# Kernel optimization log

Hardware: AMD Instinct MI355X
Metric: run time of the kernel (lower is better)

## Reference

```python
import jax, jax.numpy as jnp
import numpy as np

B = 4        # number of point clouds (equal-size contiguous batches)
P = 8192     # points per cloud
C_IN = 64
C_OUT = 64
K = 16       # kNN neighbors (includes the point itself, as in PyG knn)
EPS = 1e-5
NEG_SLOPE = 0.2


def setup_inputs() -> dict:
    key = jax.random.key(0)
    k1, k2, k3 = jax.random.split(key, 3)
    x = jax.random.normal(k1, (B * P, C_IN), dtype=jnp.float32)
    batch = jnp.repeat(jnp.arange(B, dtype=jnp.int64), P)  # sorted, equal sizes
    W = jax.random.normal(k2, (2 * C_IN, C_OUT), dtype=jnp.float32) * (1.0 / np.sqrt(2 * C_IN))
    b = jax.random.normal(k3, (C_OUT,), dtype=jnp.float32) * 0.01
    gamma = jnp.ones((C_OUT,), dtype=jnp.float32)
    beta = jnp.zeros((C_OUT,), dtype=jnp.float32)
    return {"x": x, "batch": batch, "W": W, "b": b, "gamma": gamma, "beta": beta}


def _edgeconv(x, W, b, gamma, beta):
    xb = x.reshape(B, P, C_IN)
    # per-cloud pairwise squared distances: [B, P, P]
    sq = jnp.sum(xb * xb, axis=-1)
    d = sq[:, :, None] + sq[:, None, :] - 2.0 * jnp.einsum("bpc,bqc->bpq", xb, xb)
    # k nearest neighbors (smallest distance, self included)
    _, idx = jax.lax.top_k(-d, K)                      # [B, P, K]
    xj = jax.vmap(lambda pts, ind: pts[ind])(xb, idx)  # [B, P, K, C_IN]
    xi = xb[:, :, None, :]
    e = jnp.concatenate([jnp.broadcast_to(xi, xj.shape), xj - xi], axis=-1)  # [B,P,K,2C]
    # edge MLP: Linear -> BatchNorm1d (training-mode batch stats over all edges) -> LeakyReLU
    h = jnp.einsum("bpke,eo->bpko", e, W) + b          # [B, P, K, C_OUT]
    hf = h.reshape(-1, C_OUT)
    mean = jnp.mean(hf, axis=0)
    var = jnp.mean(hf * hf, axis=0) - mean * mean      # biased variance (torch BN)
    hn = (h - mean) * jax.lax.rsqrt(var + EPS) * gamma + beta
    a = jnp.where(hn >= 0, hn, NEG_SLOPE * hn)
    # max aggregation over neighbors
    return jnp.max(a, axis=2).reshape(B * P, C_OUT)


def reference(x, batch, W, b, gamma, beta):
    # `batch` encodes B equal-size contiguous clouds; kNN is computed per cloud.
    return _edgeconv(x, W, b, gamma, beta)
```

## Files before the change

### kernel.cpp

```cpp
#include <hip/hip_runtime.h>
#include <cfloat>

#define BATCH 4
#define P 8192
#define C 64
#define KNN 16
#define NPTS (BATCH * P)
#define NEDGE (NPTS * KNN)
#define EPSV 1e-5f
#define SLOPE 0.2f
#define CAP 16

typedef __attribute__((ext_vector_type(8))) short bf16x8;
typedef __attribute__((ext_vector_type(16))) float f32x16;


__device__ __forceinline__ unsigned short f2bf(float f) {
    unsigned u = __float_as_uint(f);
    u += 0x7FFFu + ((u >> 16) & 1u);
    return (unsigned short)(u >> 16);
}
__device__ __forceinline__ float bf2f(unsigned short s) {
    return __uint_as_float(((unsigned)s) << 16);
}

__global__ void prep_frag(const float* __restrict__ x, uint4* __restrict__ xfh,
                          uint4* __restrict__ xfm, uint4* __restrict__ xfl,
                          float* __restrict__ sq) {
    __shared__ float part[32][9];
    int tid = threadIdx.x;
    int ptl = tid >> 3, j8 = tid & 7;
    int g = blockIdx.x;
    int p = g * 32 + ptl;
    const float4* xp = (const float4*)(x + (size_t)p * C + j8 * 8);
    float4 a = xp[0], b = xp[1];
    float v[8] = {a.x, a.y, a.z, a.w, b.x, b.y, b.z, b.w};
    unsigned short hs[8], ms[8], ls[8];
    float ssum = 0.f;
#pragma unroll
    for (int e = 0; e < 8; ++e) {
        float xv = v[e];
        ssum = fmaf(xv, xv, ssum);
        unsigned short h = f2bf(xv);
        float r1 = xv - bf2f(h);
        unsigned short m = f2bf(r1);
        float r2 = r1 - bf2f(m);
        unsigned short l = f2bf(r2);
        hs[e] = h; ms[e] = m; ls[e] = l;
    }
    int dst = (g * 4 + (j8 >> 1)) * 64 + ptl + 32 * (j8 & 1);
    uint4 ph, pm, pl;
    ph.x = (unsigned)hs[0] | ((unsigned)hs[1] << 16);
    ph.y = (unsigned)hs[2] | ((unsigned)hs[3] << 16);
    ph.z = (unsigned)hs[4] | ((unsigned)hs[5] << 16);
    ph.w = (unsigned)hs[6] | ((unsigned)hs[7] << 16);
    pm.x = (unsigned)ms[0] | ((unsigned)ms[1] << 16);
    pm.y = (unsigned)ms[2] | ((unsigned)ms[3] << 16);
    pm.z = (unsigned)ms[4] | ((unsigned)ms[5] << 16);
    pm.w = (unsigned)ms[6] | ((unsigned)ms[7] << 16);
    pl.x = (unsigned)ls[0] | ((unsigned)ls[1] << 16);
    pl.y = (unsigned)ls[2] | ((unsigned)ls[3] << 16);
    pl.z = (unsigned)ls[4] | ((unsigned)ls[5] << 16);
    pl.w = (unsigned)ls[6] | ((unsigned)ls[7] << 16);
    xfh[dst] = ph; xfm[dst] = pm; xfl[dst] = pl;
    part[ptl][j8] = ssum;
    __syncthreads();
    if (j8 == 0) {
        float s = 0.f;
#pragma unroll
        for (int k = 0; k < 8; ++k) s += part[ptl][k];
        sq[p] = s;
    }
}

__device__ __forceinline__ void tk_insert(float (&v)[16], int (&id)[16],
                                          float& worst, float s, int cand) {
    if (s < worst) {
        float w = v[0];
        int pos = 0;
#pragma unroll
        for (int j = 1; j < 16; ++j) {
            bool g = v[j] > w;
            w = g ? v[j] : w;
            pos = g ? j : pos;
        }
#pragma unroll
        for (int j = 0; j < 16; ++j) {
            if (j == pos) { v[j] = s; id[j] = cand; }
        }
        float nw = v[0];
#pragma unroll
        for (int j = 1; j < 16; ++j) nw = fmaxf(nw, v[j]);
        worst = nw;
    }
}

__global__ __launch_bounds__(256, 2) void knn_kernel(const uint4* __restrict__ xfh,
                                                     const uint4* __restrict__ xfm,
                                                     const uint4* __restrict__ xfl,
                                                     const float* __restrict__ sq,
                                                     int* __restrict__ idx_out) {
    __shared__ float scoresL[64 * 65];
    __shared__ float bufv[64 * 17];
    __shared__ int   bufi[64 * 17];
    __shared__ int   cntL[64];
    __shared__ float worstL[64];

    int tid = threadIdx.x;
    int b = blockIdx.x & 3;
    int tile = blockIdx.x >> 2;
    int bglob = b * P;
    int r0 = tile * 64;
    int w = tid >> 6, lane = tid & 63;
    int wr = w & 1, wc = w >> 1;

    if (tid < 64) { cntL[tid] = 0; worstL[tid] = FLT_MAX; }

    int gA = ((bglob + r0) >> 5) + wr;
    bf16x8 Ah[4], Am[4], Al[4];
#pragma unroll
    for (int kk = 0; kk < 4; ++kk) {
        Ah[kk] = __builtin_bit_cast(bf16x8, xfh[(gA * 4 + kk) * 64 + lane]);
        Am[kk] = __builtin_bit_cast(bf16x8, xfm[(gA * 4 + kk) * 64 + lane]);
        Al[kk] = __builtin_bit_cast(bf16x8, xfl[(gA * 4 + kk) * 64 + lane]);
    }

    float tv[16];
    int ti[16];
    float worst = FLT_MAX;
#pragma unroll
    for (int j = 0; j < 16; ++j) { tv[j] = FLT_MAX; ti[j] = 0; }
    int rown = ((lane & 15) << 2) | w;
    bool owner = (lane < 16);

    int selr = tid & 63;
    int selq = tid >> 6;

    for (int chunk = 0; chunk < P / 64; ++chunk) {
        int c0 = chunk * 64;
        int gB = ((bglob + c0) >> 5) + wc;
        bf16x8 Bh[4], Bm[4], Bl[4];
#pragma unroll
        for (int kk = 0; kk < 4; ++kk) {
            Bh[kk] = __builtin_bit_cast(bf16x8, xfh[(gB * 4 + kk) * 64 + lane]);
            Bm[kk] = __builtin_bit_cast(bf16x8, xfm[(gB * 4 + kk) * 64 + lane]);
            Bl[kk] = __builtin_bit_cast(bf16x8, xfl[(gB * 4 + kk) * 64 + lane]);
        }
        float sc = sq[bglob + c0 + wc * 32 + (lane & 31)];

        f32x16 acc0, acc1;
#pragma unroll
        for (int i = 0; i < 16; ++i) { acc0[i] = 0.f; acc1[i] = 0.f; }
#pragma unroll
        for (int kk = 0; kk < 4; ++kk) {
            acc0 = __builtin_amdgcn_mfma_f32_32x32x16_bf16(Ah[kk], Bh[kk], acc0, 0, 0, 0);
            acc1 = __builtin_amdgcn_mfma_f32_32x32x16_bf16(Ah[kk], Bm[kk], acc1, 0, 0, 0);
            acc0 = __builtin_amdgcn_mfma_f32_32x32x16_bf16(Am[kk], Bh[kk], acc0, 0, 0, 0);
            acc1 = __builtin_amdgcn_mfma_f32_32x32x16_bf16(Am[kk], Bm[kk], acc1, 0, 0, 0);
            acc0 = __builtin_amdgcn_mfma_f32_32x32x16_bf16(Ah[kk], Bl[kk], acc0, 0, 0, 0);
            acc1 = __builtin_amdgcn_mfma_f32_32x32x16_bf16(Al[kk], Bh[kk], acc1, 0, 0, 0);
        }

        __syncthreads();
        {
            int colL = wc * 32 + (lane & 31);
            int rbase = wr * 32 + 4 * (lane >> 5);
#pragma unroll
            for (int reg = 0; reg < 16; ++reg) {
                int row = rbase + (reg & 3) + 8 * (reg >> 2);
                scoresL[row * 65 + colL] = fmaf(-2.f, acc0[reg] + acc1[reg], sc);
            }
        }
        __syncthreads();
        {
            float wst = worstL[selr];
#pragma unroll
            for (int j = 0; j < 16; ++j) {
                float s = scoresL[selr * 65 + selq * 16 + j];
                if (s < wst) {
                    int slot = atomicAdd(&cntL[selr], 1);
                    if (slot < CAP) {
                        bufv[selr * 17 + slot] = s;
                        bufi[selr * 17 + slot] = c0 + selq * 16 + j;
                    }
                }
            }
        }
        __syncthreads();
        if (owner) {
            int n = cntL[rown];
            if (n > 0) {
                if (n > CAP) {
                    for (int e = 0; e < 64; ++e)
                        tk_insert(tv, ti, worst, scoresL[rown * 65 + e], c0 + e);
                } else {
                    for (int k = 0; k < n; ++k)
                        tk_insert(tv, ti, worst, bufv[rown * 17 + k], bufi[rown * 17 + k]);
                }
                cntL[rown] = 0;
                worstL[rown] = worst;
            }
        }
    }

    if (owner) {
        size_t o = ((size_t)(bglob + r0 + rown)) * KNN;
#pragma unroll
        for (int j = 0; j < 16; ++j) idx_out[o + j] = bglob + ti[j];
    }
}

__global__ void prep_UV(const float* __restrict__ x, const float* __restrict__ W,
                        float* __restrict__ U, float* __restrict__ V) {
    __shared__ float Ws[128][64];
    __shared__ float xs[4][64];
    int tid = threadIdx.x;
    for (int i = tid; i < 128 * 64; i += 256) ((float*)Ws)[i] = W[i];
    int p0 = blockIdx.x * 4;
    int r = tid >> 6, c = tid & 63;
    xs[r][c] = x[(size_t)(p0 + r) * C + c];
    __syncthreads();
    float u = 0.f, v = 0.f;
#pragma unroll
    for (int k = 0; k < 64; ++k) {
        float xv = xs[r][k];
        float w1 = Ws[k][c];
        float w2 = Ws[64 + k][c];
        u = fmaf(xv, w1 - w2, u);
        v = fmaf(xv, w2, v);
    }
    size_t o = (size_t)(p0 + r) * C + c;
    U[o] = u;
    V[o] = v;
}

__global__ void stats_kernel(const float* __restrict__ U, const float* __restrict__ V,
                             const float* __restrict__ bias, const int* __restrict__ idx,
                             float* __restrict__ stats) {
    int tid = threadIdx.x;
    int c = tid & 63, kk = tid >> 6;
    int p0 = blockIdx.x * 32;
    float bc = bias[c];
    float sum = 0.f, sumsq = 0.f;
    for (int pp = 0; pp < 32; ++pp) {
        int p = p0 + pp;
        float u = U[(size_t)p * C + c] + bc;
#pragma unroll
        for (int k4 = 0; k4 < 4; ++k4) {
            int j = idx[(size_t)p * KNN + kk * 4 + k4];
            float h = u + V[(size_t)j * C + c];
            sum += h;
            sumsq = fmaf(h, h, sumsq);
        }
    }
    __shared__ float red[2][4][64];
    red[0][kk][c] = sum;
    red[1][kk][c] = sumsq;
    __syncthreads();
    if (tid < 64) {
        float s = red[0][0][tid] + red[0][1][tid] + red[0][2][tid] + red[0][3][tid];
        atomicAdd(&stats[tid], s);
    } else if (tid < 128) {
        int cc = tid - 64;
        float s = red[1][0][cc] + red[1][1][cc] + red[1][2][cc] + red[1][3][cc];
        atomicAdd(&stats[64 + cc], s);
    }
}

__global__ void finalize_kernel(const float* __restrict__ stats,
                                const float* __restrict__ gamma,
                                const float* __restrict__ beta,
                                float* __restrict__ sshift) {
    int c = threadIdx.x;
    const float N = (float)NEDGE;
    float mean = stats[c] / N;
    float var = stats[64 + c] / N - mean * mean;
    float s = gamma[c] * rsqrtf(var + EPSV);
    sshift[c] = s;
    sshift[64 + c] = beta[c] - mean * s;
}

__global__ void out_kernel(const float* __restrict__ U, const float* __restrict__ V,
                           const float* __restrict__ bias, const int* __restrict__ idx,
                           const float* __restrict__ sshift, float* __restrict__ out) {
    int tid = threadIdx.x;
    int c = tid & 63, g = tid >> 6;
    int p0 = blockIdx.x * 16;
    float s = sshift[c], t = sshift[64 + c];
    float bc = bias[c];
    for (int pp = g; pp < 16; pp += 4) {
        int p = p0 + pp;
        float mx = -FLT_MAX, mn = FLT_MAX;
#pragma unroll
        for (int k = 0; k < KNN; ++k) {
            int j = idx[(size_t)p * KNN + k];
            float v = V[(size_t)j * C + c];
            mx = fmaxf(mx, v);
            mn = fminf(mn, v);
        }
        float hsel = (s >= 0.f) ? mx : mn;
        float hn = fmaf(s, U[(size_t)p * C + c] + bc + hsel, t);
        out[(size_t)p * C + c] = (hn >= 0.f) ? hn : SLOPE * hn;
    }
}

extern "C" void kernel_launch(void* const* d_in, const int* in_sizes, int n_in,
                              void* d_out, int out_size, void* d_ws, size_t ws_size,
                              hipStream_t stream) {
    const float* x     = (const float*)d_in[0];
    const float* W     = (const float*)d_in[2];
    const float* bias  = (const float*)d_in[3];
    const float* gamma = (const float*)d_in[4];
    const float* beta  = (const float*)d_in[5];
    float* out = (float*)d_out;

    float* wsf    = (float*)d_ws;
    float* U      = wsf;
    float* V      = wsf + 2097152;
    uint4* xfh    = (uint4*)wsf;
    uint4* xfm    = (uint4*)(wsf + 1048576);
    uint4* xfl    = (uint4*)(wsf + 2097152);
    float* sq     = wsf + 4194304;
    float* stats  = wsf + 4227072;
    float* sshift = wsf + 4227200;
    int*   idx    = (int*)(wsf + 4227328);

    hipLaunchKernelGGL(prep_frag, dim3(NPTS / 32), dim3(256), 0, stream, x, xfh, xfm, xfl, sq);
    hipLaunchKernelGGL(knn_kernel, dim3(BATCH * (P / 64)), dim3(256), 0, stream,
                       (const uint4*)xfh, (const uint4*)xfm, (const uint4*)xfl, sq, idx);
    hipLaunchKernelGGL(prep_UV, dim3(NPTS / 4), dim3(256), 0, stream, x, W, U, V);
    hipMemsetAsync(stats, 0, 128 * sizeof(float), stream);
    hipLaunchKernelGGL(stats_kernel, dim3(NPTS / 32), dim3(256), 0, stream, U, V, bias, idx, stats);
    hipLaunchKernelGGL(finalize_kernel, dim3(1), dim3(64), 0, stream, stats, gamma, beta, sshift);
    hipLaunchKernelGGL(out_kernel, dim3(NPTS / 16), dim3(256), 0, stream, U, V, bias, idx, sshift, out);
}
```

Measured before the change: 590.1 us.

## Split kNN column range into quarters and merge partial top-k lists

The kNN kernel now splits each row tile's candidate columns into four quarters, each handled by its own block. Each block writes a partial top-16 of distances and indices to workspace, and a new merge kernel combines the four partial lists per point. The grid before had only 512 blocks, which underfilled the GPU, so this raises the block count fourfold, and launch bounds are raised to allow more resident blocks. The cost is an extra kernel launch, extra global traffic for the partial lists, and possible register pressure from the tighter launch bound.

```diff
diff --git a/kernel.cpp b/kernel.cpp
--- a/kernel.cpp
+++ b/kernel.cpp
@@ -10,6 +10,8 @@
 #define EPSV 1e-5f
 #define SLOPE 0.2f
 #define CAP 16
+#define NQ 4
+#define QCOLS (P / NQ)
 
 typedef __attribute__((ext_vector_type(8))) short bf16x8;
 typedef __attribute__((ext_vector_type(16))) float f32x16;
@@ -95,11 +97,12 @@
     }
 }
 
-__global__ __launch_bounds__(256, 2) void knn_kernel(const uint4* __restrict__ xfh,
+__global__ __launch_bounds__(256, 6) void knn_kernel(const uint4* __restrict__ xfh,
                                                      const uint4* __restrict__ xfm,
                                                      const uint4* __restrict__ xfl,
                                                      const float* __restrict__ sq,
-                                                     int* __restrict__ idx_out) {
+                                                     float* __restrict__ pv,
+                                                     int* __restrict__ pi) {
     __shared__ float scoresL[64 * 65];
     __shared__ float bufv[64 * 17];
     __shared__ int   bufi[64 * 17];
@@ -108,9 +111,12 @@
 
     int tid = threadIdx.x;
     int b = blockIdx.x & 3;
-    int tile = blockIdx.x >> 2;
+    int t = blockIdx.x >> 2;
+    int tile = t & 127;
+    int quarter = t >> 7;
     int bglob = b * P;
     int r0 = tile * 64;
+    int colbase = quarter * QCOLS;
     int w = tid >> 6, lane = tid & 63;
     int wr = w & 1, wc = w >> 1;
 
@@ -136,8 +142,8 @@
     int selr = tid & 63;
     int selq = tid >> 6;
 
-    for (int chunk = 0; chunk < P / 64; ++chunk) {
-        int c0 = chunk * 64;
+    for (int chunk = 0; chunk < QCOLS / 64; ++chunk) {
+        int c0 = colbase + chunk * 64;
         int gB = ((bglob + c0) >> 5) + wc;
         bf16x8 Bh[4], Bm[4], Bl[4];
 #pragma unroll
@@ -204,9 +210,40 @@
     }
 
     if (owner) {
-        size_t o = ((size_t)(bglob + r0 + rown)) * KNN;
-#pragma unroll
-        for (int j = 0; j < 16; ++j) idx_out[o + j] = bglob + ti[j];
+        size_t o = (((size_t)(bglob + r0 + rown)) * NQ + quarter) * KNN;
+#pragma unroll
+        for (int j = 0; j < 16; ++j) {
+            pv[o + j] = tv[j];
+            pi[o + j] = bglob + ti[j];
+        }
+    }
+}
+
+__global__ void merge_kernel(const float* __restrict__ pv, const int* __restrict__ pi,
+                             int* __restrict__ idx_out) {
+    __shared__ float mv[64][65];
+    __shared__ int   mi[64][65];
+    int tid = threadIdx.x;
+    int lr = tid & 63, q = tid >> 6;
+    int row = blockIdx.x * 64 + lr;
+    size_t o = ((size_t)row * NQ + q) * KNN;
+#pragma unroll
+    for (int j = 0; j < 16; ++j) {
+        mv[lr][q * 16 + j] = pv[o + j];
+        mi[lr][q * 16 + j] = pi[o + j];
+    }
+    __syncthreads();
+    if (tid < 64) {
+        float tv[16];
+        int ti[16];
+        float worst = FLT_MAX;
+#pragma unroll
+        for (int j = 0; j < 16; ++j) { tv[j] = FLT_MAX; ti[j] = 0; }
+        for (int e = 0; e < 64; ++e)
+            tk_insert(tv, ti, worst, mv[tid][e], mi[tid][e]);
+        size_t oo = (size_t)row * KNN;
+#pragma unroll
+        for (int j = 0; j < 16; ++j) idx_out[oo + j] = ti[j];
     }
 }
 
@@ -324,10 +361,13 @@
     float* stats  = wsf + 4227072;
     float* sshift = wsf + 4227200;
     int*   idx    = (int*)(wsf + 4227328);
+    float* pv     = wsf + 4751616;
+    int*   pi     = (int*)(wsf + 6848768);
 
     hipLaunchKernelGGL(prep_frag, dim3(NPTS / 32), dim3(256), 0, stream, x, xfh, xfm, xfl, sq);
-    hipLaunchKernelGGL(knn_kernel, dim3(BATCH * (P / 64)), dim3(256), 0, stream,
-                       (const uint4*)xfh, (const uint4*)xfm, (const uint4*)xfl, sq, idx);
+    hipLaunchKernelGGL(knn_kernel, dim3(BATCH * (P / 64) * NQ), dim3(256), 0, stream,
+                       (const uint4*)xfh, (const uint4*)xfm, (const uint4*)xfl, sq, pv, pi);
+    hipLaunchKernelGGL(merge_kernel, dim3(NPTS / 64), dim3(256), 0, stream, pv, pi, idx);
     hipLaunchKernelGGL(prep_UV, dim3(NPTS / 4), dim3(256), 0, stream, x, W, U, V);
     hipMemsetAsync(stats, 0, 128 * sizeof(float), stream);
     hipLaunchKernelGGL(stats_kernel, dim3(NPTS / 32), dim3(256), 0, stream, U, V, bias, idx, stats);
```

Result: slower. 1.114 ms (+88.8%).
